# Optimization experiments

Hardware: AMD Instinct MI355X
Metric: run time of the kernel (lower is better)

## Reference

```python
import jax, jax.numpy as jnp
import numpy as np

N_NODES = 50000
N_EDGES = 800000
IN_DIM = 256
HID = 64
HEADS = 4
OUT_DIM = 16
N_GRAPHS = 64
NEG_SLOPE = 0.2


def setup_inputs() -> dict:
    key = jax.random.key(0)
    ks = jax.random.split(key, 16)
    H2 = HID // 2  # conv2 out channels (heads=1, concat=False)
    H4 = HID // 4
    inp = {
        "x": jax.random.normal(ks[0], (N_NODES, IN_DIM), jnp.float32),
        "edge_index": jax.random.randint(ks[1], (2, N_EDGES), 0, N_NODES, jnp.int64),
        "batch": jnp.sort(jax.random.randint(ks[2], (N_NODES,), 0, N_GRAPHS, jnp.int64)),
        # GATConv 1: in=IN_DIM, out=HID, heads=HEADS, concat=True
        "W1": jax.random.normal(ks[3], (IN_DIM, HEADS * HID), jnp.float32) * 0.05,
        "att_src1": jax.random.normal(ks[4], (HEADS, HID), jnp.float32) * 0.1,
        "att_dst1": jax.random.normal(ks[5], (HEADS, HID), jnp.float32) * 0.1,
        "b1": jnp.zeros((HEADS * HID,), jnp.float32),
        # GATConv 2: in=HEADS*HID, out=HID/2, heads=1, concat=False
        "W2": jax.random.normal(ks[6], (HEADS * HID, H2), jnp.float32) * 0.05,
        "att_src2": jax.random.normal(ks[7], (1, H2), jnp.float32) * 0.1,
        "att_dst2": jax.random.normal(ks[8], (1, H2), jnp.float32) * 0.1,
        "b2": jnp.zeros((H2,), jnp.float32),
        "fc1_w": jax.random.normal(ks[9], (H2, H4), jnp.float32) * 0.1,
        "fc1_b": jnp.zeros((H4,), jnp.float32),
        "fc2_w": jax.random.normal(ks[10], (H4, OUT_DIM), jnp.float32) * 0.1,
        "fc2_b": jnp.zeros((OUT_DIM,), jnp.float32),
    }
    return inp


def gat_conv(x, W, att_src, att_dst, bias, src, dst, num_nodes, concat):
    """PyG-style GATConv (eval mode, self-loops already in src/dst)."""
    H, C = att_src.shape
    h = (x @ W).reshape(num_nodes, H, C)          # [N,H,C]
    a_src = (h * att_src).sum(-1)                 # [N,H]
    a_dst = (h * att_dst).sum(-1)                 # [N,H]
    e = jax.nn.leaky_relu(a_src[src] + a_dst[dst], NEG_SLOPE)  # [E,H]
    # segment softmax over destination nodes (self-loops => every segment nonempty)
    emax = jax.ops.segment_max(e, dst, num_segments=num_nodes)
    ex = jnp.exp(e - emax[dst])
    denom = jax.ops.segment_sum(ex, dst, num_segments=num_nodes)
    alpha = ex / (denom[dst] + 1e-16)             # [E,H]
    msg = h[src] * alpha[:, :, None]              # [E,H,C]
    out = jax.ops.segment_sum(msg, dst, num_segments=num_nodes)  # [N,H,C]
    out = out.reshape(num_nodes, H * C) if concat else out.mean(axis=1)
    return out + bias


def reference(x, edge_index, batch, W1, att_src1, att_dst1, b1,
              W2, att_src2, att_dst2, b2, fc1_w, fc1_b, fc2_w, fc2_b):
    num_nodes = x.shape[0]
    loops = jnp.arange(num_nodes, dtype=edge_index.dtype)
    src = jnp.concatenate([edge_index[0], loops])
    dst = jnp.concatenate([edge_index[1], loops])

    h = gat_conv(x, W1, att_src1, att_dst1, b1, src, dst, num_nodes, concat=True)
    h = jax.nn.relu(h)                                 # dropout: eval no-op
    h = gat_conv(h, W2, att_src2, att_dst2, b2, src, dst, num_nodes, concat=False)

    # global mean pool over graphs
    sums = jax.ops.segment_sum(h, batch, num_segments=N_GRAPHS)
    cnts = jax.ops.segment_sum(jnp.ones((num_nodes,), h.dtype), batch, num_segments=N_GRAPHS)
    g = sums / jnp.maximum(cnts, 1.0)[:, None]         # [G, HID/2]

    g = jax.nn.relu(g)
    g = jax.nn.relu(g @ fc1_w + fc1_b)
    g = jax.nn.relu(g @ fc2_w + fc2_b)
    return g
```

## Files before the change

kernel.cpp:

```cpp
#include <hip/hip_runtime.h>
#include <math.h>

#define NEG 0.2f
#define LMAX 1024
#define CAP 1600
typedef unsigned short u16;
typedef unsigned int u32;
typedef __bf16 bf16x8 __attribute__((ext_vector_type(8)));
typedef float f32x4 __attribute__((ext_vector_type(4)));

__device__ __forceinline__ float bf2f(u16 u) {
    union { unsigned i; float f; } x; x.i = ((unsigned)u) << 16; return x.f;
}
__device__ __forceinline__ u16 f2bf(float f) {
    union { float f; unsigned u; } x; x.f = f;
    unsigned r = x.u + 0x7fffu + ((x.u >> 16) & 1u);
    return (u16)(r >> 16);
}

__global__ void zero_i32(int* __restrict__ p, int n) {
    int i = blockIdx.x * blockDim.x + threadIdx.x;
    if (i < n) p[i] = 0;
}

__global__ __launch_bounds__(256) void bkt_scatter_pad(const int* __restrict__ ei,
                                                       int* __restrict__ bktcur,
                                                       u32* __restrict__ ebuf,
                                                       int E, int ET, int NBK) {
    __shared__ int lcnt[LMAX];
    __shared__ int lbase[LMAX];
    int t = threadIdx.x;
    for (int b = t; b < NBK; b += 256) lcnt[b] = 0;
    __syncthreads();
    int base = blockIdx.x * 8192;
    for (int k = 0; k < 32; ++k) {
        int i = base + k * 256 + t;
        if (i < ET) {
            int d = (i < E) ? ei[E + i] : (i - E);
            atomicAdd(&lcnt[d >> 6], 1);
        }
    }
    __syncthreads();
    for (int b = t; b < NBK; b += 256) {
        int c = lcnt[b];
        lbase[b] = c ? (b * CAP + atomicAdd(&bktcur[b], c)) : 0;
    }
    __syncthreads();
    for (int b = t; b < NBK; b += 256) lcnt[b] = 0;
    __syncthreads();
    for (int k = 0; k < 32; ++k) {
        int i = base + k * 256 + t;
        if (i < ET) {
            int s, d;
            if (i < E) { s = ei[i]; d = ei[E + i]; }
            else       { s = i - E; d = s; }
            int b = d >> 6;
            int idx = atomicAdd(&lcnt[b], 1);
            ebuf[lbase[b] + idx] = (u32)s | ((u32)(d & 63) << 16);
        }
    }
}

__global__ __launch_bounds__(256) void bucket_csr_pad(const u32* __restrict__ ebuf,
                                                      const int* __restrict__ bktcur,
                                                      int* __restrict__ row_ptr,
                                                      int* __restrict__ rowend,
                                                      int* __restrict__ col, int N) {
    __shared__ int cnt[64];
    __shared__ int cur[64];
    int b = blockIdx.x, t = threadIdx.x;
    int v0 = b << 6;
    int s0 = b * CAP, s1 = s0 + bktcur[b];
    if (t < 64) cnt[t] = 0;
    __syncthreads();
    for (int i = s0 + t; i < s1; i += 256)
        atomicAdd(&cnt[(ebuf[i] >> 16) & 63], 1);
    __syncthreads();
    if (t < 64) {
        int c = cnt[t];
        int val = c;
#pragma unroll
        for (int off = 1; off < 64; off <<= 1) {
            int n = __shfl_up(val, off, 64);
            if (t >= off) val += n;
        }
        int excl = s0 + val - c;
        if (v0 + t < N) { row_ptr[v0 + t] = excl; rowend[v0 + t] = excl + c; }
        cur[t] = excl;
    }
    __syncthreads();
    for (int i = s0 + t; i < s1; i += 256) {
        u32 v = ebuf[i];
        int pos = atomicAdd(&cur[(v >> 16) & 63], 1);
        col[pos] = (int)(v & 0xFFFFu);
    }
}

__global__ void prep_w1(const float* __restrict__ W1, const float* __restrict__ att_s,
                        const float* __restrict__ att_d, u16* __restrict__ w1x) {
    int k = blockIdx.x;
    int c = threadIdx.x;
    float w = W1[k * 256 + c];
    w1x[c * 256 + k] = f2bf(w);
    int head = c >> 6;
    float vs = w * att_s[c];
    float vd = w * att_d[c];
#pragma unroll
    for (int mask = 1; mask < 64; mask <<= 1) {
        vs += __shfl_xor(vs, mask, 64);
        vd += __shfl_xor(vd, mask, 64);
    }
    if ((c & 63) == 0) {
        w1x[(256 + head) * 256 + k] = f2bf(vs);
        w1x[(260 + head) * 256 + k] = f2bf(vd);
        w1x[(264 + head) * 256 + k] = 0;
        w1x[(268 + head) * 256 + k] = 0;
    }
}

__global__ __launch_bounds__(512) void gemm1_lds(const float* __restrict__ x,
                                                 const u16* __restrict__ w1x,
                                                 u16* __restrict__ h1b,
                                                 float* __restrict__ asad, int N) {
    __shared__ __align__(16) u16 wl[272 * 264];
    for (int f = threadIdx.x; f < 272 * 32; f += 512) {
        int r = f >> 5, cc = f & 31;
        *reinterpret_cast<uint4*>(&wl[r * 264 + cc * 8]) =
            *reinterpret_cast<const uint4*>(w1x + r * 256 + cc * 8);
    }
    __syncthreads();

    int wave = threadIdx.x >> 6, lane = threadIdx.x & 63;
    int g = lane >> 4, l15 = lane & 15;
    int ntiles = (N + 15) >> 4;
    for (int tile = blockIdx.x * 8 + wave; tile < ntiles; tile += gridDim.x * 8) {
        int r0 = tile << 4;
        int arow = r0 + l15; if (arow > N - 1) arow = N - 1;
        const float* xp = x + (size_t)arow * 256 + g * 8;

        f32x4 acc[17];
#pragma unroll
        for (int n = 0; n < 17; ++n) acc[n] = (f32x4){0.f, 0.f, 0.f, 0.f};

#pragma unroll
        for (int ks = 0; ks < 8; ++ks) {
            float4 a0 = *reinterpret_cast<const float4*>(xp + ks * 32);
            float4 a1 = *reinterpret_cast<const float4*>(xp + ks * 32 + 4);
            bf16x8 af;
            af[0] = (__bf16)a0.x; af[1] = (__bf16)a0.y; af[2] = (__bf16)a0.z; af[3] = (__bf16)a0.w;
            af[4] = (__bf16)a1.x; af[5] = (__bf16)a1.y; af[6] = (__bf16)a1.z; af[7] = (__bf16)a1.w;
#pragma unroll
            for (int n = 0; n < 17; ++n) {
                bf16x8 bf = *reinterpret_cast<const bf16x8*>(&wl[(n * 16 + l15) * 264 + ks * 32 + g * 8]);
                acc[n] = __builtin_amdgcn_mfma_f32_16x16x32_bf16(af, bf, acc[n], 0, 0, 0);
            }
        }

#pragma unroll
        for (int reg = 0; reg < 4; ++reg) {
            int grow = r0 + g * 4 + reg;
            if (grow < N) {
#pragma unroll
                for (int n = 0; n < 16; ++n)
                    h1b[(size_t)grow * 256 + n * 16 + l15] = f2bf(acc[n][reg]);
                if (l15 < 8) asad[(size_t)grow * 8 + l15] = acc[16][reg];
            }
        }
    }
}

__global__ __launch_bounds__(256) void conv1_fused(const u16* __restrict__ h1b,
                                                   const float* __restrict__ asad,
                                                   const int* __restrict__ row_ptr,
                                                   const int* __restrict__ rowend,
                                                   const int* __restrict__ col,
                                                   const float* __restrict__ b1,
                                                   u16* __restrict__ hin2b, int N) {
    __shared__ float la[4][128][4];
    __shared__ int   lc[4][128];
    int idx = blockIdx.x * blockDim.x + threadIdx.x;
    int v = idx >> 6; if (v > N - 1) v = N - 1;
    int lane = idx & 63;
    int node = threadIdx.x >> 6;
    int head = lane >> 4, l15 = lane & 15;
    float adst = asad[(size_t)v * 8 + 4 + head];
    int beg = row_ptr[v], end = rowend[v];
    int deg = end - beg;
    bool fast = (deg <= 128);
    float m = -1e30f, l = 0.f;
    if (fast) {
        float e[8]; int u[8];
#pragma unroll
        for (int i = 0; i < 8; ++i) {
            int p = beg + l15 + i * 16;
            float ev = -1e30f; int uu = 0;
            if (p < end) {
                uu = col[p];
                float tv = asad[(size_t)uu * 8 + head] + adst;
                ev = tv > 0.f ? tv : NEG * tv;
            }
            e[i] = ev; u[i] = uu;
        }
        m = e[0];
#pragma unroll
        for (int i = 1; i < 8; ++i) m = fmaxf(m, e[i]);
#pragma unroll
        for (int mask = 1; mask < 16; mask <<= 1) m = fmaxf(m, __shfl_xor(m, mask, 64));
#pragma unroll
        for (int i = 0; i < 8; ++i) {
            int j = l15 + i * 16;
            if (beg + j < end) {
                float a = __expf(e[i] - m);
                l += a;
                la[node][j][head] = a;
                if (head == 0) lc[node][j] = u[i];
            }
        }
#pragma unroll
        for (int mask = 1; mask < 16; mask <<= 1) l += __shfl_xor(l, mask, 64);
    } else {
        for (int p = beg + l15; p < end; p += 16) {
            float tv = asad[(size_t)col[p] * 8 + head] + adst;
            tv = tv > 0.f ? tv : NEG * tv;
            m = fmaxf(m, tv);
        }
#pragma unroll
        for (int mask = 1; mask < 16; mask <<= 1) m = fmaxf(m, __shfl_xor(m, mask, 64));
        for (int p = beg + l15; p < end; p += 16) {
            float tv = asad[(size_t)col[p] * 8 + head] + adst;
            tv = tv > 0.f ? tv : NEG * tv;
            l += __expf(tv - m);
        }
#pragma unroll
        for (int mask = 1; mask < 16; mask <<= 1) l += __shfl_xor(l, mask, 64);
    }
    __syncthreads();
    float inv = 1.f / (l + 1e-16f);

    float ax = 0.f, ay = 0.f, az = 0.f, aw = 0.f;
    if (fast) {
        int j = 0;
        for (; j + 3 < deg; j += 4) {
            float a0 = la[node][j + 0][head];
            float a1 = la[node][j + 1][head];
            float a2 = la[node][j + 2][head];
            float a3 = la[node][j + 3][head];
            int u0 = lc[node][j + 0], u1 = lc[node][j + 1];
            int u2 = lc[node][j + 2], u3 = lc[node][j + 3];
            ushort4 h0 = *reinterpret_cast<const ushort4*>(h1b + (size_t)u0 * 256 + lane * 4);
            ushort4 h1 = *reinterpret_cast<const ushort4*>(h1b + (size_t)u1 * 256 + lane * 4);
            ushort4 h2 = *reinterpret_cast<const ushort4*>(h1b + (size_t)u2 * 256 + lane * 4);
            ushort4 h3 = *reinterpret_cast<const ushort4*>(h1b + (size_t)u3 * 256 + lane * 4);
            ax += a0 * bf2f(h0.x) + a1 * bf2f(h1.x) + a2 * bf2f(h2.x) + a3 * bf2f(h3.x);
            ay += a0 * bf2f(h0.y) + a1 * bf2f(h1.y) + a2 * bf2f(h2.y) + a3 * bf2f(h3.y);
            az += a0 * bf2f(h0.z) + a1 * bf2f(h1.z) + a2 * bf2f(h2.z) + a3 * bf2f(h3.z);
            aw += a0 * bf2f(h0.w) + a1 * bf2f(h1.w) + a2 * bf2f(h2.w) + a3 * bf2f(h3.w);
        }
        for (; j < deg; ++j) {
            float a = la[node][j][head];
            int u = lc[node][j];
            ushort4 hv = *reinterpret_cast<const ushort4*>(h1b + (size_t)u * 256 + lane * 4);
            ax += a * bf2f(hv.x);
            ay += a * bf2f(hv.y);
            az += a * bf2f(hv.z);
            aw += a * bf2f(hv.w);
        }
    } else {
        for (int p = beg; p < end; ++p) {
            int u = col[p];
            float tv = asad[(size_t)u * 8 + head] + adst;
            tv = tv > 0.f ? tv : NEG * tv;
            float a = __expf(tv - m);
            ushort4 hv = *reinterpret_cast<const ushort4*>(h1b + (size_t)u * 256 + lane * 4);
            ax += a * bf2f(hv.x);
            ay += a * bf2f(hv.y);
            az += a * bf2f(hv.z);
            aw += a * bf2f(hv.w);
        }
    }
    int c = lane * 4;
    ushort4 o;
    o.x = f2bf(fmaxf(ax * inv + b1[c + 0], 0.f));
    o.y = f2bf(fmaxf(ay * inv + b1[c + 1], 0.f));
    o.z = f2bf(fmaxf(az * inv + b1[c + 2], 0.f));
    o.w = f2bf(fmaxf(aw * inv + b1[c + 3], 0.f));
    *reinterpret_cast<ushort4*>(hin2b + (size_t)v * 256 + c) = o;
}

__global__ __launch_bounds__(256) void gemm2_att(const u16* __restrict__ hin2b,
                                                 const float* __restrict__ W2,
                                                 const float* __restrict__ att_s,
                                                 const float* __restrict__ att_d,
                                                 u16* __restrict__ h2b, float* __restrict__ as2,
                                                 float* __restrict__ ad2, int N) {
    __shared__ __align__(16) float ws2[256 * 32];
    int t = threadIdx.x;
#pragma unroll
    for (int i = 0; i < 8; ++i) {
        int f4 = i * 256 + t;
        *reinterpret_cast<float4*>(ws2 + f4 * 4) = *reinterpret_cast<const float4*>(W2 + f4 * 4);
    }
    __syncthreads();
    int half = t >> 5, j = t & 31;
    int nb = blockIdx.x * 64 + half * 8;
    float acc[8] = {};
    int nmax = N - 1;
    for (int k0 = 0; k0 < 256; k0 += 8) {
        float w[8];
#pragma unroll
        for (int i = 0; i < 8; ++i) w[i] = ws2[(k0 + i) * 32 + j];
#pragma unroll
        for (int q = 0; q < 8; ++q) {
            int nc = nb + q; nc = nc > nmax ? nmax : nc;
            uint4 hv = *reinterpret_cast<const uint4*>(hin2b + (size_t)nc * 256 + k0);
            acc[q] += bf2f((u16)(hv.x & 0xffff)) * w[0] + bf2f((u16)(hv.x >> 16)) * w[1]
                    + bf2f((u16)(hv.y & 0xffff)) * w[2] + bf2f((u16)(hv.y >> 16)) * w[3]
                    + bf2f((u16)(hv.z & 0xffff)) * w[4] + bf2f((u16)(hv.z >> 16)) * w[5]
                    + bf2f((u16)(hv.w & 0xffff)) * w[6] + bf2f((u16)(hv.w >> 16)) * w[7];
        }
    }
    float asj = att_s[j], adj = att_d[j];
#pragma unroll
    for (int q = 0; q < 8; ++q) {
        int n = nb + q;
        bool ok = n < N;
        float a = acc[q];
        if (ok) h2b[(size_t)n * 32 + j] = f2bf(a);
        float vs = a * asj, vd = a * adj;
#pragma unroll
        for (int mask = 1; mask < 32; mask <<= 1) {
            vs += __shfl_xor(vs, mask, 64);
            vd += __shfl_xor(vd, mask, 64);
        }
        if (j == 0 && ok) { as2[n] = vs; ad2[n] = vd; }
    }
}

__global__ __launch_bounds__(256) void conv2_fused(const u16* __restrict__ h2b,
                                                   const float* __restrict__ as2,
                                                   const float* __restrict__ ad2,
                                                   const int* __restrict__ row_ptr,
                                                   const int* __restrict__ rowend,
                                                   const int* __restrict__ col,
                                                   const float* __restrict__ b2,
                                                   float* __restrict__ out2, int N) {
    __shared__ float la[8][128];
    __shared__ int   lc[8][128];
    int idx = blockIdx.x * blockDim.x + threadIdx.x;
    int v = idx >> 5; if (v > N - 1) v = N - 1;
    int lane = idx & 31;
    int node = threadIdx.x >> 5;
    float adst = ad2[v];
    int beg = row_ptr[v], end = rowend[v];
    int deg = end - beg;
    bool fast = (deg <= 128);
    float m = -1e30f, l = 0.f;
    if (fast) {
        float e[4]; int u[4];
#pragma unroll
        for (int i = 0; i < 4; ++i) {
            int p = beg + lane + i * 32;
            float ev = -1e30f; int uu = 0;
            if (p < end) {
                uu = col[p];
                float tv = as2[uu] + adst;
                ev = tv > 0.f ? tv : NEG * tv;
            }
            e[i] = ev; u[i] = uu;
        }
        m = fmaxf(fmaxf(e[0], e[1]), fmaxf(e[2], e[3]));
#pragma unroll
        for (int mask = 1; mask < 32; mask <<= 1) m = fmaxf(m, __shfl_xor(m, mask, 64));
#pragma unroll
        for (int i = 0; i < 4; ++i) {
            int j = lane + i * 32;
            if (beg + j < end) {
                float a = __expf(e[i] - m);
                l += a;
                la[node][j] = a;
                lc[node][j] = u[i];
            }
        }
#pragma unroll
        for (int mask = 1; mask < 32; mask <<= 1) l += __shfl_xor(l, mask, 64);
    } else {
        for (int p = beg + lane; p < end; p += 32) {
            float tv = as2[col[p]] + adst;
            tv = tv > 0.f ? tv : NEG * tv;
            m = fmaxf(m, tv);
        }
#pragma unroll
        for (int mask = 1; mask < 32; mask <<= 1) m = fmaxf(m, __shfl_xor(m, mask, 64));
        for (int p = beg + lane; p < end; p += 32) {
            float tv = as2[col[p]] + adst;
            tv = tv > 0.f ? tv : NEG * tv;
            l += __expf(tv - m);
        }
#pragma unroll
        for (int mask = 1; mask < 32; mask <<= 1) l += __shfl_xor(l, mask, 64);
    }
    __syncthreads();
    float inv = 1.f / (l + 1e-16f);

    float acc = 0.f;
    if (fast) {
        int j = 0;
        for (; j + 3 < deg; j += 4) {
            float a0 = la[node][j + 0], a1 = la[node][j + 1];
            float a2 = la[node][j + 2], a3 = la[node][j + 3];
            int u0 = lc[node][j + 0], u1 = lc[node][j + 1];
            int u2 = lc[node][j + 2], u3 = lc[node][j + 3];
            acc += a0 * bf2f(h2b[(size_t)u0 * 32 + lane])
                 + a1 * bf2f(h2b[(size_t)u1 * 32 + lane])
                 + a2 * bf2f(h2b[(size_t)u2 * 32 + lane])
                 + a3 * bf2f(h2b[(size_t)u3 * 32 + lane]);
        }
        for (; j < deg; ++j)
            acc += la[node][j] * bf2f(h2b[(size_t)lc[node][j] * 32 + lane]);
    } else {
        for (int p = beg; p < end; ++p) {
            int u = col[p];
            float tv = as2[u] + adst;
            tv = tv > 0.f ? tv : NEG * tv;
            acc += __expf(tv - m) * bf2f(h2b[(size_t)u * 32 + lane]);
        }
    }
    out2[(size_t)v * 32 + lane] = acc * inv + b2[lane];
}

__global__ __launch_bounds__(256) void pool_fc(const float* __restrict__ out2,
                                               const int* __restrict__ batch,
                                               const float* __restrict__ fc1w,
                                               const float* __restrict__ fc1b,
                                               const float* __restrict__ fc2w,
                                               const float* __restrict__ fc2b,
                                               float* __restrict__ out, int N) {
    int g = blockIdx.x;
    int lo = 0, hi = N;
    while (lo < hi) { int mid = (lo + hi) >> 1; if (batch[mid] < g) lo = mid + 1; else hi = mid; }
    int s = lo;
    lo = 0; hi = N;
    while (lo < hi) { int mid = (lo + hi) >> 1; if (batch[mid] < g + 1) lo = mid + 1; else hi = mid; }
    int e = lo;

    int c = threadIdx.x & 31, grp = threadIdx.x >> 5;
    float sum = 0.f;
    for (int r = s + grp; r < e; r += 8) sum += out2[(size_t)r * 32 + c];
    __shared__ float part[8][32];
    part[grp][c] = sum;
    __syncthreads();
    __shared__ float g0[32];
    if (grp == 0) {
        float tot = 0.f;
#pragma unroll
        for (int q = 0; q < 8; ++q) tot += part[q][c];
        float cnt = (float)(e - s);
        g0[c] = fmaxf(tot / fmaxf(cnt, 1.0f), 0.f);
    }
    __syncthreads();
    __shared__ float z1[16];
    if (threadIdx.x < 16) {
        float a = fc1b[threadIdx.x];
        for (int k = 0; k < 32; ++k) a += g0[k] * fc1w[k * 16 + threadIdx.x];
        z1[threadIdx.x] = fmaxf(a, 0.f);
    }
    __syncthreads();
    if (threadIdx.x < 16) {
        float a = fc2b[threadIdx.x];
        for (int k = 0; k < 16; ++k) a += z1[k] * fc2w[k * 16 + threadIdx.x];
        out[g * 16 + threadIdx.x] = fmaxf(a, 0.f);
    }
}

extern "C" void kernel_launch(void* const* d_in, const int* in_sizes, int n_in,
                              void* d_out, int out_size, void* d_ws, size_t ws_size,
                              hipStream_t stream) {
    const float* x      = (const float*)d_in[0];
    const int*   ei     = (const int*)d_in[1];
    const int*   batch  = (const int*)d_in[2];
    const float* W1     = (const float*)d_in[3];
    const float* att_s1 = (const float*)d_in[4];
    const float* att_d1 = (const float*)d_in[5];
    const float* b1     = (const float*)d_in[6];
    const float* W2     = (const float*)d_in[7];
    const float* att_s2 = (const float*)d_in[8];
    const float* att_d2 = (const float*)d_in[9];
    const float* b2     = (const float*)d_in[10];
    const float* fc1w   = (const float*)d_in[11];
    const float* fc1b   = (const float*)d_in[12];
    const float* fc2w   = (const float*)d_in[13];
    const float* fc2b   = (const float*)d_in[14];
    float* out = (float*)d_out;

    int N = in_sizes[0] / 256;
    int E = in_sizes[1] / 2;
    int ET = E + N;
    int NBK = (N + 63) >> 6;
    int nchunks = (ET + 8191) / 8192;

    char* ws = (char*)d_ws;
    size_t off = 0;
    auto alloc = [&](size_t bytes) { size_t o = off; off = (off + bytes + 255) & ~255ULL; return o; };
    u16*  w1x    = (u16*)(ws + alloc(272 * 256 * 2));
    u16*  h1b    = (u16*)(ws + alloc((size_t)N * 256 * 2));
    float* asad  = (float*)(ws + alloc((size_t)N * 8 * 4));
    u16*  hin2b  = (u16*)(ws + alloc((size_t)N * 256 * 2));
    u16*  h2b    = (u16*)(ws + alloc((size_t)N * 32 * 2));
    float* as2   = (float*)(ws + alloc((size_t)N * 4));
    float* ad2   = (float*)(ws + alloc((size_t)N * 4));
    float* out2  = (float*)(ws + alloc((size_t)N * 32 * 4));
    int* row_ptr = (int*)(ws + alloc((size_t)N * 4));
    int* rowend  = (int*)(ws + alloc((size_t)N * 4));
    int* col     = (int*)(ws + alloc((size_t)NBK * CAP * 4));
    int* bktcur  = (int*)(ws + alloc((size_t)NBK * 4));
    u32* ebuf    = (u32*)(ws + alloc((size_t)NBK * CAP * 4));
    (void)ws_size; (void)n_in; (void)out_size;

    prep_w1<<<256, 256, 0, stream>>>(W1, att_s1, att_d1, w1x);

    zero_i32<<<(NBK + 255) / 256, 256, 0, stream>>>(bktcur, NBK);
    bkt_scatter_pad<<<nchunks, 256, 0, stream>>>(ei, bktcur, ebuf, E, ET, NBK);
    bucket_csr_pad<<<NBK, 256, 0, stream>>>(ebuf, bktcur, row_ptr, rowend, col, N);

    gemm1_lds<<<256, 512, 0, stream>>>(x, w1x, h1b, asad, N);
    conv1_fused<<<(N * 64 + 255) / 256, 256, 0, stream>>>(h1b, asad, row_ptr, rowend, col, b1, hin2b, N);

    gemm2_att<<<(N + 63) / 64, 256, 0, stream>>>(hin2b, W2, att_s2, att_d2, h2b, as2, ad2, N);
    conv2_fused<<<(N * 32 + 255) / 256, 256, 0, stream>>>(h2b, as2, ad2, row_ptr, rowend, col, b2, out2, N);

    pool_fc<<<64, 256, 0, stream>>>(out2, batch, fc1w, fc1b, fc2w, fc2b, out, N);
}
```

Before: 226.4 us.

## Replace scalar conv2 GEMM with bf16 MFMA kernel folding attention projections

The second-layer GEMM moves from scalar FMA loops to bf16 MFMA 16x16x32 instructions, with W2 pre-converted to bf16 and transposed in a small prep kernel. The attention source and destination vectors are folded into extra weight rows, so as2 and ad2 come out of the same MFMA instead of a shuffle reduction. This removes scalar compute and LDS float traffic. The cost is one extra tiny launch and reduced precision, since W2 and the folded attention weights are now rounded to bf16.

```diff
diff --git a/kernel.cpp b/kernel.cpp
--- a/kernel.cpp
+++ b/kernel.cpp
@@ -116,6 +116,23 @@
         w1x[(264 + head) * 256 + k] = 0;
         w1x[(268 + head) * 256 + k] = 0;
     }
+}
+
+__global__ void prep_w2(const float* __restrict__ W2, const float* __restrict__ att_s,
+                        const float* __restrict__ att_d, u16* __restrict__ w2x) {
+    int k = threadIdx.x;
+    float a_s = 0.f, a_d = 0.f;
+#pragma unroll
+    for (int j = 0; j < 32; ++j) {
+        float w = W2[k * 32 + j];
+        w2x[j * 256 + k] = f2bf(w);
+        a_s += w * att_s[j];
+        a_d += w * att_d[j];
+    }
+    w2x[32 * 256 + k] = f2bf(a_s);
+    w2x[33 * 256 + k] = f2bf(a_d);
+#pragma unroll
+    for (int r = 34; r < 48; ++r) w2x[r * 256 + k] = 0;
 }
 
 __global__ __launch_bounds__(512) void gemm1_lds(const float* __restrict__ x,
@@ -287,52 +304,51 @@
     *reinterpret_cast<ushort4*>(hin2b + (size_t)v * 256 + c) = o;
 }
 
-__global__ __launch_bounds__(256) void gemm2_att(const u16* __restrict__ hin2b,
-                                                 const float* __restrict__ W2,
-                                                 const float* __restrict__ att_s,
-                                                 const float* __restrict__ att_d,
-                                                 u16* __restrict__ h2b, float* __restrict__ as2,
-                                                 float* __restrict__ ad2, int N) {
-    __shared__ __align__(16) float ws2[256 * 32];
-    int t = threadIdx.x;
-#pragma unroll
-    for (int i = 0; i < 8; ++i) {
-        int f4 = i * 256 + t;
-        *reinterpret_cast<float4*>(ws2 + f4 * 4) = *reinterpret_cast<const float4*>(W2 + f4 * 4);
-    }
-    __syncthreads();
-    int half = t >> 5, j = t & 31;
-    int nb = blockIdx.x * 64 + half * 8;
-    float acc[8] = {};
-    int nmax = N - 1;
-    for (int k0 = 0; k0 < 256; k0 += 8) {
-        float w[8];
-#pragma unroll
-        for (int i = 0; i < 8; ++i) w[i] = ws2[(k0 + i) * 32 + j];
-#pragma unroll
-        for (int q = 0; q < 8; ++q) {
-            int nc = nb + q; nc = nc > nmax ? nmax : nc;
-            uint4 hv = *reinterpret_cast<const uint4*>(hin2b + (size_t)nc * 256 + k0);
-            acc[q] += bf2f((u16)(hv.x & 0xffff)) * w[0] + bf2f((u16)(hv.x >> 16)) * w[1]
-                    + bf2f((u16)(hv.y & 0xffff)) * w[2] + bf2f((u16)(hv.y >> 16)) * w[3]
-                    + bf2f((u16)(hv.z & 0xffff)) * w[4] + bf2f((u16)(hv.z >> 16)) * w[5]
-                    + bf2f((u16)(hv.w & 0xffff)) * w[6] + bf2f((u16)(hv.w >> 16)) * w[7];
-        }
-    }
-    float asj = att_s[j], adj = att_d[j];
-#pragma unroll
-    for (int q = 0; q < 8; ++q) {
-        int n = nb + q;
-        bool ok = n < N;
-        float a = acc[q];
-        if (ok) h2b[(size_t)n * 32 + j] = f2bf(a);
-        float vs = a * asj, vd = a * adj;
-#pragma unroll
-        for (int mask = 1; mask < 32; mask <<= 1) {
-            vs += __shfl_xor(vs, mask, 64);
-            vd += __shfl_xor(vd, mask, 64);
-        }
-        if (j == 0 && ok) { as2[n] = vs; ad2[n] = vd; }
+__global__ __launch_bounds__(512) void gemm2_mfma(const u16* __restrict__ hin2b,
+                                                  const u16* __restrict__ w2x,
+                                                  u16* __restrict__ h2b,
+                                                  float* __restrict__ as2,
+                                                  float* __restrict__ ad2, int N) {
+    __shared__ __align__(16) u16 wl[48 * 264];
+    for (int f = threadIdx.x; f < 48 * 32; f += 512) {
+        int r = f >> 5, cc = f & 31;
+        *reinterpret_cast<uint4*>(&wl[r * 264 + cc * 8]) =
+            *reinterpret_cast<const uint4*>(w2x + r * 256 + cc * 8);
+    }
+    __syncthreads();
+
+    int wave = threadIdx.x >> 6, lane = threadIdx.x & 63;
+    int g = lane >> 4, l15 = lane & 15;
+    int ntiles = (N + 15) >> 4;
+    for (int tile = blockIdx.x * 8 + wave; tile < ntiles; tile += gridDim.x * 8) {
+        int r0 = tile << 4;
+        int arow = r0 + l15; if (arow > N - 1) arow = N - 1;
+        const u16* hp = hin2b + (size_t)arow * 256 + g * 8;
+
+        f32x4 acc[3];
+#pragma unroll
+        for (int n = 0; n < 3; ++n) acc[n] = (f32x4){0.f, 0.f, 0.f, 0.f};
+
+#pragma unroll
+        for (int ks = 0; ks < 8; ++ks) {
+            bf16x8 af = *reinterpret_cast<const bf16x8*>(hp + ks * 32);
+#pragma unroll
+            for (int n = 0; n < 3; ++n) {
+                bf16x8 bf = *reinterpret_cast<const bf16x8*>(&wl[(n * 16 + l15) * 264 + ks * 32 + g * 8]);
+                acc[n] = __builtin_amdgcn_mfma_f32_16x16x32_bf16(af, bf, acc[n], 0, 0, 0);
+            }
+        }
+
+#pragma unroll
+        for (int reg = 0; reg < 4; ++reg) {
+            int grow = r0 + g * 4 + reg;
+            if (grow < N) {
+                h2b[(size_t)grow * 32 + l15]      = f2bf(acc[0][reg]);
+                h2b[(size_t)grow * 32 + 16 + l15] = f2bf(acc[1][reg]);
+                if (l15 == 0) as2[grow] = acc[2][reg];
+                if (l15 == 1) ad2[grow] = acc[2][reg];
+            }
+        }
     }
 }
 
@@ -502,6 +518,7 @@
     size_t off = 0;
     auto alloc = [&](size_t bytes) { size_t o = off; off = (off + bytes + 255) & ~255ULL; return o; };
     u16*  w1x    = (u16*)(ws + alloc(272 * 256 * 2));
+    u16*  w2x    = (u16*)(ws + alloc(48 * 256 * 2));
     u16*  h1b    = (u16*)(ws + alloc((size_t)N * 256 * 2));
     float* asad  = (float*)(ws + alloc((size_t)N * 8 * 4));
     u16*  hin2b  = (u16*)(ws + alloc((size_t)N * 256 * 2));
@@ -517,6 +534,7 @@
     (void)ws_size; (void)n_in; (void)out_size;
 
     prep_w1<<<256, 256, 0, stream>>>(W1, att_s1, att_d1, w1x);
+    prep_w2<<<1, 256, 0, stream>>>(W2, att_s2, att_d2, w2x);
 
     zero_i32<<<(NBK + 255) / 256, 256, 0, stream>>>(bktcur, NBK);
     bkt_scatter_pad<<<nchunks, 256, 0, stream>>>(ei, bktcur, ebuf, E, ET, NBK);
@@ -525,7 +543,7 @@
     gemm1_lds<<<256, 512, 0, stream>>>(x, w1x, h1b, asad, N);
     conv1_fused<<<(N * 64 + 255) / 256, 256, 0, stream>>>(h1b, asad, row_ptr, rowend, col, b1, hin2b, N);
 
-    gemm2_att<<<(N + 63) / 64, 256, 0, stream>>>(hin2b, W2, att_s2, att_d2, h2b, as2, ad2, N);
+    gemm2_mfma<<<256, 512, 0, stream>>>(hin2b, w2x, h2b, as2, ad2, N);
     conv2_fused<<<(N * 32 + 255) / 256, 256, 0, stream>>>(h2b, as2, ad2, row_ptr, rowend, col, b2, out2, N);
 
     pool_fc<<<64, 256, 0, stream>>>(out2, batch, fc1w, fc1b, fc2w, fc2b, out, N);
```

Result: faster. 199.3 us (-12.0%).
